# Optimization experiments

Measured on AMD Instinct MI355X. Metric: run time of the kernel, lower is better.

## Reference

```python
import jax, jax.numpy as jnp
import numpy as np

B, N, H = 2, 2048, 256
NUM_HEADS = 8
HEAD_DIM = H // NUM_HEADS
E = 65536
NEG = -1e30
LN_EPS = 1e-5


def setup_inputs() -> dict:
    key = jax.random.key(0)
    ks = jax.random.split(key, 8)
    x = jax.random.normal(ks[0], (B, N, H), dtype=jnp.float32)
    edge_index = jax.random.randint(ks[1], (2, E), 0, N, dtype=jnp.int32)
    edge_weights = jax.random.uniform(ks[2], (E,), dtype=jnp.float32)
    s = 1.0 / np.sqrt(H)
    Wq = jax.random.normal(ks[3], (H, H), dtype=jnp.float32) * s
    Wk = jax.random.normal(ks[4], (H, H), dtype=jnp.float32) * s
    Wv = jax.random.normal(ks[5], (H, H), dtype=jnp.float32) * s
    Wo = jax.random.normal(ks[6], (H, H), dtype=jnp.float32) * s
    ln_gamma = jnp.ones((H,), dtype=jnp.float32)
    ln_beta = jnp.zeros((H,), dtype=jnp.float32)
    return {"node_embeddings": x, "edge_index": edge_index, "edge_weights": edge_weights,
            "Wq": Wq, "Wk": Wk, "Wv": Wv, "Wo": Wo, "ln_gamma": ln_gamma, "ln_beta": ln_beta}


def reference(node_embeddings, edge_index, edge_weights, Wq, Wk, Wv, Wo, ln_gamma, ln_beta):
    x = node_embeddings
    residual = x
    # torch Linear: y = x @ W.T
    def proj(W):
        y = jnp.einsum('bnd,ed->bne', x, W)
        return y.reshape(B, N, NUM_HEADS, HEAD_DIM).transpose(0, 2, 1, 3)  # [B,h,N,hd]
    Q, K, V = proj(Wq), proj(Wk), proj(Wv)
    scale = 1.0 / jnp.sqrt(jnp.float32(HEAD_DIM))
    scores = jnp.einsum('bhnd,bhmd->bhnm', Q, K) * scale  # [B,h,N,N]
    # adjacency mask from edge list
    mask = jnp.zeros((N, N), dtype=bool).at[edge_index[0], edge_index[1]].set(True)
    scores = jnp.where(mask[None, None], scores, NEG)
    w = jax.nn.softmax(scores, axis=-1)
    # rows with no edges: softmax over uniform NEG -> uniform; multiply by mask zeroes them
    # (equivalent to torch's -inf softmax + nan->0, but grad-safe)
    w = w * mask[None, None].astype(w.dtype)
    attn = jnp.einsum('bhnm,bhmd->bhnd', w, V)
    attn = attn.transpose(0, 2, 1, 3).reshape(B, N, H)
    out = jnp.einsum('bnd,ed->bne', attn, Wo)
    y = out + residual
    mu = jnp.mean(y, axis=-1, keepdims=True)
    var = jnp.mean(jnp.square(y - mu), axis=-1, keepdims=True)
    y = (y - mu) / jnp.sqrt(var + LN_EPS) * ln_gamma + ln_beta
    return y
```

## Files before the change

### kernel.cpp

```cpp
#include <hip/hip_runtime.h>
#include <math.h>

#define Bb 2
#define Nn 2048
#define Hh 256
#define NH 8
#define HD 32
#define NEDGE 65536
#define LN_EPS 1e-5f
#define MW 64

typedef __bf16 bf16_t;
typedef bf16_t bf16x8 __attribute__((ext_vector_type(8)));
typedef bf16_t bf16x4 __attribute__((ext_vector_type(4)));
typedef float f32x4 __attribute__((ext_vector_type(4)));

__global__ void build_mask_kernel(const int* __restrict__ ei, unsigned int* __restrict__ mask) {
    int e = blockIdx.x * blockDim.x + threadIdx.x;
    if (e >= NEDGE) return;
    int src = ei[e];
    int dst = ei[NEDGE + e];
    atomicOr(&mask[src * MW + (dst >> 5)], 1u << (dst & 31));
}

#define LDA2 72

__global__ __launch_bounds__(256) void qkv_gemm3_kernel(
    const float* __restrict__ x,
    const float* __restrict__ Wq, const float* __restrict__ Wk, const float* __restrict__ Wv,
    float* __restrict__ Qb, bf16_t* __restrict__ Kb16, bf16_t* __restrict__ Vb16)
{
    __shared__ bf16_t As[64 * LDA2];
    __shared__ bf16_t Ws[64 * LDA2];
    int t = threadIdx.x;
    int lane = t & 63, w = t >> 6;
    int wm = w & 1, wn = w >> 1;
    int ml = lane & 15, quad = lane >> 4;
    int m0 = blockIdx.x * 64;
    int wsel = blockIdx.y >> 2;
    const float* W = (wsel == 0) ? Wq : ((wsel == 1) ? Wk : Wv);
    int n0 = (blockIdx.y & 3) * 64;
    int srow = t >> 3;
    int scol = (t & 7) * 8;
    f32x4 acc[2][2];
    f32x4 zero = {0.f, 0.f, 0.f, 0.f};
    acc[0][0] = zero; acc[0][1] = zero; acc[1][0] = zero; acc[1][1] = zero;

    for (int k0 = 0; k0 < Hh; k0 += 64) {
        float4 a[2][2], bwt[2][2];
        #pragma unroll
        for (int s = 0; s < 2; ++s) {
            const float* ap = x + (size_t)(m0 + srow + s * 32) * Hh + k0 + scol;
            a[s][0] = *(const float4*)ap;
            a[s][1] = *(const float4*)(ap + 4);
            const float* bp = W + (size_t)(n0 + srow + s * 32) * Hh + k0 + scol;
            bwt[s][0] = *(const float4*)bp;
            bwt[s][1] = *(const float4*)(bp + 4);
        }
        __syncthreads();
        #pragma unroll
        for (int s = 0; s < 2; ++s) {
            bf16x8 av = {(bf16_t)a[s][0].x, (bf16_t)a[s][0].y, (bf16_t)a[s][0].z, (bf16_t)a[s][0].w,
                         (bf16_t)a[s][1].x, (bf16_t)a[s][1].y, (bf16_t)a[s][1].z, (bf16_t)a[s][1].w};
            bf16x8 bv = {(bf16_t)bwt[s][0].x, (bf16_t)bwt[s][0].y, (bf16_t)bwt[s][0].z, (bf16_t)bwt[s][0].w,
                         (bf16_t)bwt[s][1].x, (bf16_t)bwt[s][1].y, (bf16_t)bwt[s][1].z, (bf16_t)bwt[s][1].w};
            *(bf16x8*)&As[(srow + s * 32) * LDA2 + scol] = av;
            *(bf16x8*)&Ws[(srow + s * 32) * LDA2 + scol] = bv;
        }
        __syncthreads();
        #pragma unroll
        for (int kk = 0; kk < 64; kk += 32) {
            bf16x8 af[2], bfr[2];
            #pragma unroll
            for (int i = 0; i < 2; ++i) {
                af[i]  = *(const bf16x8*)&As[(wm * 32 + i * 16 + ml) * LDA2 + kk + quad * 8];
                bfr[i] = *(const bf16x8*)&Ws[(wn * 32 + i * 16 + ml) * LDA2 + kk + quad * 8];
            }
            #pragma unroll
            for (int i = 0; i < 2; ++i)
                #pragma unroll
                for (int j = 0; j < 2; ++j)
                    acc[i][j] = __builtin_amdgcn_mfma_f32_16x16x32_bf16(af[i], bfr[j], acc[i][j], 0, 0, 0);
        }
    }
    bf16_t* Ob16 = (wsel == 1) ? Kb16 : Vb16;
    #pragma unroll
    for (int i = 0; i < 2; ++i)
        #pragma unroll
        for (int j = 0; j < 2; ++j)
            #pragma unroll
            for (int r = 0; r < 4; ++r) {
                int mg = m0 + wm * 32 + i * 16 + quad * 4 + r;
                int ng = n0 + wn * 32 + j * 16 + ml;
                float v = acc[i][j][r];
                if (wsel == 0) Qb[(size_t)mg * Hh + ng] = v;
                else           Ob16[(size_t)mg * Hh + ng] = (bf16_t)v;
            }
}

__global__ __launch_bounds__(256) void attn6_kernel(
    const float* __restrict__ Qb, const bf16_t* __restrict__ Kb16, const bf16_t* __restrict__ Vb16,
    const unsigned int* __restrict__ mask, float* __restrict__ attnb)
{
    __shared__ unsigned short nbr[Nn];
    __shared__ float qs[2][Hh];
    __shared__ float sraw[2][32 * 9];
    __shared__ float scw[2][Hh];
    __shared__ float alpha_l[2][NH];
    __shared__ float linv_l[2][NH];
    __shared__ float obuf[4][Hh];
    __shared__ int nn_sh;
    int i = blockIdx.x;
    int t = threadIdx.x;
    int h = t >> 5, dl = t & 31;
    int w = t >> 6, lane = t & 63;
    int hw = lane >> 3;

    if (t < 64) {
        unsigned int bits = mask[i * MW + t];
        int cnt = __popc(bits);
        int incl = cnt;
        #pragma unroll
        for (int off = 1; off < 64; off <<= 1) {
            int v = __shfl_up(incl, off, 64);
            if (t >= off) incl += v;
        }
        int idx = incl - cnt;
        unsigned int bb = bits;
        while (bb) {
            int bit = __ffs(bb) - 1;
            nbr[idx++] = (unsigned short)(t * 32 + bit);
            bb &= bb - 1;
        }
        if (t == 63) nn_sh = incl;
    }
    qs[0][t] = Qb[(size_t)i * Hh + t];
    qs[1][t] = Qb[(size_t)(Nn + i) * Hh + t];
    __syncthreads();
    int nn = nn_sh;

    float m_run[2] = {-1e30f, -1e30f};
    float l_run[2] = {0.f, 0.f};
    float o[2][4] = {{0.f, 0.f, 0.f, 0.f}, {0.f, 0.f, 0.f, 0.f}};
    const float scale = 0.17677669529663687f;
    int nch = (nn + 31) >> 5;
    for (int c = 0; c < nch; ++c) {
        int base = c << 5;
        int lim = min(32, nn - base);
        #pragma unroll
        for (int b = 0; b < 2; ++b) {
            float4 qv = *(const float4*)&qs[b][lane << 2];
            #pragma unroll
            for (int s = 0; s < 8; ++s) {
                int r = (s << 2) + w;
                if (r < lim) {
                    int j = nbr[base + r];
                    bf16x4 kv = *(const bf16x4*)(Kb16 + (((size_t)((b << 11) + j)) << 8) + (lane << 2));
                    float p = fmaf((float)kv.x, qv.x, fmaf((float)kv.y, qv.y,
                              fmaf((float)kv.z, qv.z, (float)kv.w * qv.w)));
                    p += __shfl_xor(p, 1, 64);
                    p += __shfl_xor(p, 2, 64);
                    p += __shfl_xor(p, 4, 64);
                    if ((lane & 7) == 0) sraw[b][r * 9 + (lane >> 3)] = p * scale;
                }
            }
        }
        __syncthreads();
        #pragma unroll
        for (int b = 0; b < 2; ++b) {
            float s_val = (dl < lim) ? sraw[b][dl * 9 + h] : -1e30f;
            float mc = s_val;
            #pragma unroll
            for (int m = 1; m < 32; m <<= 1) mc = fmaxf(mc, __shfl_xor(mc, m, 64));
            float m_new = fmaxf(m_run[b], mc);
            float wgt = __expf(s_val - m_new);
            float sum = wgt;
            #pragma unroll
            for (int m = 1; m < 32; m <<= 1) sum += __shfl_xor(sum, m, 64);
            float alpha = __expf(m_run[b] - m_new);
            l_run[b] = l_run[b] * alpha + sum;
            m_run[b] = m_new;
            scw[b][t] = wgt;
            if (dl == 0) alpha_l[b][h] = alpha;
        }
        __syncthreads();
        #pragma unroll
        for (int b = 0; b < 2; ++b) {
            float av = alpha_l[b][hw];
            o[b][0] *= av; o[b][1] *= av; o[b][2] *= av; o[b][3] *= av;
            #pragma unroll
            for (int s = 0; s < 8; ++s) {
                int r = (s << 2) + w;
                if (r < lim) {
                    int j = nbr[base + r];
                    float wg = scw[b][(hw << 5) + r];
                    bf16x4 vv = *(const bf16x4*)(Vb16 + (((size_t)((b << 11) + j)) << 8) + (lane << 2));
                    o[b][0] = fmaf(wg, (float)vv.x, o[b][0]);
                    o[b][1] = fmaf(wg, (float)vv.y, o[b][1]);
                    o[b][2] = fmaf(wg, (float)vv.z, o[b][2]);
                    o[b][3] = fmaf(wg, (float)vv.w, o[b][3]);
                }
            }
        }
    }
    if (dl == 0) {
        linv_l[0][h] = (l_run[0] > 0.f) ? 1.f / l_run[0] : 0.f;
        linv_l[1][h] = (l_run[1] > 0.f) ? 1.f / l_run[1] : 0.f;
    }
    #pragma unroll
    for (int b = 0; b < 2; ++b) {
        __syncthreads();
        obuf[w][(lane << 2) + 0] = o[b][0];
        obuf[w][(lane << 2) + 1] = o[b][1];
        obuf[w][(lane << 2) + 2] = o[b][2];
        obuf[w][(lane << 2) + 3] = o[b][3];
        __syncthreads();
        float val = obuf[0][t] + obuf[1][t] + obuf[2][t] + obuf[3][t];
        attnb[(((size_t)((b << 11) + i)) << 8) + t] = val * linv_l[b][t >> 5];
    }
}

__global__ __launch_bounds__(256) void out_ln_kernel(
    const float* __restrict__ attnb, const float* __restrict__ Wo,
    const float* __restrict__ x, const float* __restrict__ gamma,
    const float* __restrict__ beta, float* __restrict__ out)
{
    __shared__ bf16_t As[16 * LDA2];
    __shared__ __align__(16) char wbuf[256 * LDA2 * sizeof(bf16_t)];
    bf16_t* Ws = (bf16_t*)wbuf;
    float* yb = (float*)wbuf;
    int t = threadIdx.x;
    int lane = t & 63, w = t >> 6;
    int ml = lane & 15, quad = lane >> 4;
    int m0 = blockIdx.x * 16;
    f32x4 acc[4];
    f32x4 zero = {0.f, 0.f, 0.f, 0.f};
    acc[0] = zero; acc[1] = zero; acc[2] = zero; acc[3] = zero;
    int arow = t >> 4, acol = (t & 15) * 4;
    int wrow = t >> 3, wcol = (t & 7) * 8;

    for (int k0 = 0; k0 < Hh; k0 += 64) {
        float4 av = *(const float4*)(attnb + (size_t)(m0 + arow) * Hh + k0 + acol);
        float4 wva[8], wvb[8];
        #pragma unroll
        for (int s = 0; s < 8; ++s) {
            const float* wp = Wo + (size_t)(wrow + s * 32) * Hh + k0 + wcol;
            wva[s] = *(const float4*)wp;
            wvb[s] = *(const float4*)(wp + 4);
        }
        __syncthreads();
        bf16x4 ac = {(bf16_t)av.x, (bf16_t)av.y, (bf16_t)av.z, (bf16_t)av.w};
        *(bf16x4*)&As[arow * LDA2 + acol] = ac;
        #pragma unroll
        for (int s = 0; s < 8; ++s) {
            bf16x8 wv8 = {(bf16_t)wva[s].x, (bf16_t)wva[s].y, (bf16_t)wva[s].z, (bf16_t)wva[s].w,
                          (bf16_t)wvb[s].x, (bf16_t)wvb[s].y, (bf16_t)wvb[s].z, (bf16_t)wvb[s].w};
            *(bf16x8*)&Ws[(wrow + s * 32) * LDA2 + wcol] = wv8;
        }
        __syncthreads();
        #pragma unroll
        for (int kk = 0; kk < 64; kk += 32) {
            bf16x8 af = *(const bf16x8*)&As[ml * LDA2 + kk + quad * 8];
            #pragma unroll
            for (int ct = 0; ct < 4; ++ct) {
                bf16x8 bfr = *(const bf16x8*)&Ws[(w * 64 + ct * 16 + ml) * LDA2 + kk + quad * 8];
                acc[ct] = __builtin_amdgcn_mfma_f32_16x16x32_bf16(af, bfr, acc[ct], 0, 0, 0);
            }
        }
    }
    __syncthreads();
    #pragma unroll
    for (int ct = 0; ct < 4; ++ct)
        #pragma unroll
        for (int r = 0; r < 4; ++r) {
            int row = quad * 4 + r;
            int col = w * 64 + ct * 16 + ml;
            yb[row * 260 + col] = acc[ct][r] + x[(size_t)(m0 + row) * Hh + col];
        }
    __syncthreads();
    for (int rr = 0; rr < 4; ++rr) {
        int row = w * 4 + rr;
        float4 v = *(const float4*)&yb[row * 260 + lane * 4];
        float sum = v.x + v.y + v.z + v.w;
        #pragma unroll
        for (int m = 1; m < 64; m <<= 1) sum += __shfl_xor(sum, m, 64);
        float mu = sum * (1.f / Hh);
        float4 d = {v.x - mu, v.y - mu, v.z - mu, v.w - mu};
        float ss = d.x * d.x + d.y * d.y + d.z * d.z + d.w * d.w;
        #pragma unroll
        for (int m = 1; m < 64; m <<= 1) ss += __shfl_xor(ss, m, 64);
        float r = rsqrtf(ss * (1.f / Hh) + LN_EPS);
        float4 g  = *(const float4*)(gamma + lane * 4);
        float4 bt = *(const float4*)(beta + lane * 4);
        float4 ov = {d.x * r * g.x + bt.x, d.y * r * g.y + bt.y,
                     d.z * r * g.z + bt.z, d.w * r * g.w + bt.w};
        *(float4*)(out + (size_t)(m0 + row) * Hh + lane * 4) = ov;
    }
}

extern "C" void kernel_launch(void* const* d_in, const int* in_sizes, int n_in,
                              void* d_out, int out_size, void* d_ws, size_t ws_size,
                              hipStream_t stream) {
    const float* x     = (const float*)d_in[0];
    const int*   ei    = (const int*)d_in[1];
    const float* Wq    = (const float*)d_in[3];
    const float* Wk    = (const float*)d_in[4];
    const float* Wv    = (const float*)d_in[5];
    const float* Wo    = (const float*)d_in[6];
    const float* gamma = (const float*)d_in[7];
    const float* beta  = (const float*)d_in[8];
    float* out = (float*)d_out;

    const int NTOK = Bb * Nn * Hh;
    float*  Qb    = (float*)d_ws;
    bf16_t* Kb16  = (bf16_t*)(Qb + NTOK);
    bf16_t* Vb16  = Kb16 + NTOK;
    float*  attnb = (float*)(Vb16 + NTOK);
    unsigned int* mask = (unsigned int*)(attnb + NTOK);

    hipMemsetAsync(mask, 0, Nn * MW * sizeof(unsigned int), stream);
    hipLaunchKernelGGL(build_mask_kernel, dim3(NEDGE / 256), dim3(256), 0, stream, ei, mask);
    hipLaunchKernelGGL(qkv_gemm3_kernel, dim3((Bb * Nn) / 64, 12), dim3(256), 0, stream,
                       x, Wq, Wk, Wv, Qb, Kb16, Vb16);
    hipLaunchKernelGGL(attn6_kernel, dim3(Nn), dim3(256), 0, stream,
                       Qb, Kb16, Vb16, mask, attnb);
    hipLaunchKernelGGL(out_ln_kernel, dim3((Bb * Nn) / 16), dim3(256), 0, stream,
                       attnb, Wo, x, gamma, beta, out);
}
```

Baseline: 118.6 us.

## Fuse all stages into one persistent cooperative kernel with grid syncs

Adds a single persistent cooperative kernel that runs mask clearing, mask build plus QKV GEMM, sparse attention, and output projection with LayerNorm in sequence, separated by grid-wide syncs. It replaces the memset and four separate launches. The goal is to remove launch gaps and per-kernel tail effects. In exchange, grid size is capped by occupancy, each phase loops over work units, and the grid barriers add sync cost. The fallback path also changes the attention launch grid to Bb*Nn blocks, which looks inconsistent with the fused version's per-node loop over both batches.

```diff
diff --git a/kernel.cpp b/kernel.cpp
--- a/kernel.cpp
+++ b/kernel.cpp
@@ -1,5 +1,8 @@
 #include <hip/hip_runtime.h>
+#include <hip/hip_cooperative_groups.h>
 #include <math.h>
+
+namespace cg = cooperative_groups;
 
 #define Bb 2
 #define Nn 2048
@@ -9,11 +12,304 @@
 #define NEDGE 65536
 #define LN_EPS 1e-5f
 #define MW 64
+#define LDA2 72
 
 typedef __bf16 bf16_t;
 typedef bf16_t bf16x8 __attribute__((ext_vector_type(8)));
 typedef bf16_t bf16x4 __attribute__((ext_vector_type(4)));
 typedef float f32x4 __attribute__((ext_vector_type(4)));
+
+__global__ __launch_bounds__(256, 4) void fused_kernel(
+    const float* __restrict__ x, const int* __restrict__ ei,
+    const float* __restrict__ Wq, const float* __restrict__ Wk, const float* __restrict__ Wv,
+    const float* __restrict__ Wo, const float* __restrict__ gamma, const float* __restrict__ beta,
+    float* __restrict__ Qb, bf16_t* __restrict__ Kb16, bf16_t* __restrict__ Vb16,
+    float* __restrict__ attnb, unsigned int* __restrict__ mask, float* __restrict__ out)
+{
+    __shared__ __align__(16) char smembuf[39168];
+    cg::grid_group grid = cg::this_grid();
+    const int t = threadIdx.x;
+    const int bid = blockIdx.x;
+    const int g = gridDim.x;
+    const int lane = t & 63, w = t >> 6;
+    const int ml = lane & 15, quad = lane >> 4;
+
+    {
+        uint4* m4 = (uint4*)mask;
+        const uint4 z = make_uint4(0, 0, 0, 0);
+        for (int idx = bid * 256 + t; idx < Nn * MW / 4; idx += g * 256)
+            m4[idx] = z;
+    }
+    grid.sync();
+
+    {
+        bf16_t* As = (bf16_t*)smembuf;
+        bf16_t* Ws = (bf16_t*)(smembuf + 9216);
+        const int wm = w & 1, wn = w >> 1;
+        const int srow = t >> 3, scol = (t & 7) * 8;
+        for (int u = bid; u < 1024; u += g) {
+            if (u < 768) {
+                int m0 = (u & 63) << 6;
+                int ysel = u >> 6;
+                int wsel = ysel >> 2;
+                const float* W = (wsel == 0) ? Wq : ((wsel == 1) ? Wk : Wv);
+                int n0 = (ysel & 3) << 6;
+                f32x4 acc[2][2];
+                f32x4 zero = {0.f, 0.f, 0.f, 0.f};
+                acc[0][0] = zero; acc[0][1] = zero; acc[1][0] = zero; acc[1][1] = zero;
+                for (int k0 = 0; k0 < Hh; k0 += 64) {
+                    float4 a[2][2], bwt[2][2];
+                    #pragma unroll
+                    for (int s = 0; s < 2; ++s) {
+                        const float* ap = x + (size_t)(m0 + srow + s * 32) * Hh + k0 + scol;
+                        a[s][0] = *(const float4*)ap;
+                        a[s][1] = *(const float4*)(ap + 4);
+                        const float* bp = W + (size_t)(n0 + srow + s * 32) * Hh + k0 + scol;
+                        bwt[s][0] = *(const float4*)bp;
+                        bwt[s][1] = *(const float4*)(bp + 4);
+                    }
+                    __syncthreads();
+                    #pragma unroll
+                    for (int s = 0; s < 2; ++s) {
+                        bf16x8 av = {(bf16_t)a[s][0].x, (bf16_t)a[s][0].y, (bf16_t)a[s][0].z, (bf16_t)a[s][0].w,
+                                     (bf16_t)a[s][1].x, (bf16_t)a[s][1].y, (bf16_t)a[s][1].z, (bf16_t)a[s][1].w};
+                        bf16x8 bv = {(bf16_t)bwt[s][0].x, (bf16_t)bwt[s][0].y, (bf16_t)bwt[s][0].z, (bf16_t)bwt[s][0].w,
+                                     (bf16_t)bwt[s][1].x, (bf16_t)bwt[s][1].y, (bf16_t)bwt[s][1].z, (bf16_t)bwt[s][1].w};
+                        *(bf16x8*)&As[(srow + s * 32) * LDA2 + scol] = av;
+                        *(bf16x8*)&Ws[(srow + s * 32) * LDA2 + scol] = bv;
+                    }
+                    __syncthreads();
+                    #pragma unroll
+                    for (int kk = 0; kk < 64; kk += 32) {
+                        bf16x8 af[2], bfr[2];
+                        #pragma unroll
+                        for (int i2 = 0; i2 < 2; ++i2) {
+                            af[i2]  = *(const bf16x8*)&As[(wm * 32 + i2 * 16 + ml) * LDA2 + kk + quad * 8];
+                            bfr[i2] = *(const bf16x8*)&Ws[(wn * 32 + i2 * 16 + ml) * LDA2 + kk + quad * 8];
+                        }
+                        #pragma unroll
+                        for (int i2 = 0; i2 < 2; ++i2)
+                            #pragma unroll
+                            for (int j2 = 0; j2 < 2; ++j2)
+                                acc[i2][j2] = __builtin_amdgcn_mfma_f32_16x16x32_bf16(af[i2], bfr[j2], acc[i2][j2], 0, 0, 0);
+                    }
+                }
+                bf16_t* Ob16 = (wsel == 1) ? Kb16 : Vb16;
+                #pragma unroll
+                for (int i2 = 0; i2 < 2; ++i2)
+                    #pragma unroll
+                    for (int j2 = 0; j2 < 2; ++j2)
+                        #pragma unroll
+                        for (int r = 0; r < 4; ++r) {
+                            int mg = m0 + wm * 32 + i2 * 16 + quad * 4 + r;
+                            int ng = n0 + wn * 32 + j2 * 16 + ml;
+                            float v = acc[i2][j2][r];
+                            if (wsel == 0) Qb[(size_t)mg * Hh + ng] = v;
+                            else           Ob16[(size_t)mg * Hh + ng] = (bf16_t)v;
+                        }
+            } else {
+                int e = (u - 768) * 256 + t;
+                int src = ei[e];
+                int dst = ei[NEDGE + e];
+                atomicOr(&mask[src * MW + (dst >> 5)], 1u << (dst & 31));
+            }
+        }
+    }
+    __threadfence();
+    grid.sync();
+
+    {
+        unsigned short* nbr = (unsigned short*)smembuf;
+        float* qs      = (float*)(smembuf + 4096);
+        float* sraw    = (float*)(smembuf + 6144);
+        float* scw     = (float*)(smembuf + 8448);
+        float* alpha_l = (float*)(smembuf + 10496);
+        float* linv_l  = (float*)(smembuf + 10560);
+        float* obuf    = (float*)(smembuf + 10624);
+        int*   nn_sh   = (int*)(smembuf + 14720);
+        const int h = t >> 5, dl = t & 31;
+        const int hw = lane >> 3;
+        const float scale = 0.17677669529663687f;
+
+        for (int i = bid; i < Nn; i += g) {
+            if (t < 64) {
+                unsigned int bits = mask[i * MW + t];
+                int cnt = __popc(bits);
+                int incl = cnt;
+                #pragma unroll
+                for (int off = 1; off < 64; off <<= 1) {
+                    int v = __shfl_up(incl, off, 64);
+                    if (t >= off) incl += v;
+                }
+                int idx = incl - cnt;
+                unsigned int bb = bits;
+                while (bb) {
+                    int bit = __ffs(bb) - 1;
+                    nbr[idx++] = (unsigned short)(t * 32 + bit);
+                    bb &= bb - 1;
+                }
+                if (t == 63) *nn_sh = incl;
+            }
+            qs[t]       = Qb[(size_t)i * Hh + t];
+            qs[256 + t] = Qb[(size_t)(Nn + i) * Hh + t];
+            __syncthreads();
+            int nn = *nn_sh;
+
+            float m_run[2] = {-1e30f, -1e30f};
+            float l_run[2] = {0.f, 0.f};
+            float o[2][4] = {{0.f, 0.f, 0.f, 0.f}, {0.f, 0.f, 0.f, 0.f}};
+            int nch = (nn + 31) >> 5;
+            for (int c = 0; c < nch; ++c) {
+                int base = c << 5;
+                int lim = min(32, nn - base);
+                #pragma unroll
+                for (int b = 0; b < 2; ++b) {
+                    float4 qv = *(const float4*)&qs[b * 256 + (lane << 2)];
+                    #pragma unroll
+                    for (int s = 0; s < 8; ++s) {
+                        int r = (s << 2) + w;
+                        if (r < lim) {
+                            int j = nbr[base + r];
+                            bf16x4 kv = *(const bf16x4*)(Kb16 + (((size_t)((b << 11) + j)) << 8) + (lane << 2));
+                            float p = fmaf((float)kv.x, qv.x, fmaf((float)kv.y, qv.y,
+                                      fmaf((float)kv.z, qv.z, (float)kv.w * qv.w)));
+                            p += __shfl_xor(p, 1, 64);
+                            p += __shfl_xor(p, 2, 64);
+                            p += __shfl_xor(p, 4, 64);
+                            if ((lane & 7) == 0) sraw[b * 288 + r * 9 + (lane >> 3)] = p * scale;
+                        }
+                    }
+                }
+                __syncthreads();
+                #pragma unroll
+                for (int b = 0; b < 2; ++b) {
+                    float s_val = (dl < lim) ? sraw[b * 288 + dl * 9 + h] : -1e30f;
+                    float mc = s_val;
+                    #pragma unroll
+                    for (int m = 1; m < 32; m <<= 1) mc = fmaxf(mc, __shfl_xor(mc, m, 64));
+                    float m_new = fmaxf(m_run[b], mc);
+                    float wgt = __expf(s_val - m_new);
+                    float sum = wgt;
+                    #pragma unroll
+                    for (int m = 1; m < 32; m <<= 1) sum += __shfl_xor(sum, m, 64);
+                    float alpha = __expf(m_run[b] - m_new);
+                    l_run[b] = l_run[b] * alpha + sum;
+                    m_run[b] = m_new;
+                    scw[b * 256 + t] = wgt;
+                    if (dl == 0) alpha_l[b * 8 + h] = alpha;
+                }
+                __syncthreads();
+                #pragma unroll
+                for (int b = 0; b < 2; ++b) {
+                    float av = alpha_l[b * 8 + hw];
+                    o[b][0] *= av; o[b][1] *= av; o[b][2] *= av; o[b][3] *= av;
+                    #pragma unroll
+                    for (int s = 0; s < 8; ++s) {
+                        int r = (s << 2) + w;
+                        if (r < lim) {
+                            int j = nbr[base + r];
+                            float wg = scw[b * 256 + (hw << 5) + r];
+                            bf16x4 vv = *(const bf16x4*)(Vb16 + (((size_t)((b << 11) + j)) << 8) + (lane << 2));
+                            o[b][0] = fmaf(wg, (float)vv.x, o[b][0]);
+                            o[b][1] = fmaf(wg, (float)vv.y, o[b][1]);
+                            o[b][2] = fmaf(wg, (float)vv.z, o[b][2]);
+                            o[b][3] = fmaf(wg, (float)vv.w, o[b][3]);
+                        }
+                    }
+                }
+            }
+            if (dl == 0) {
+                linv_l[h]     = (l_run[0] > 0.f) ? 1.f / l_run[0] : 0.f;
+                linv_l[8 + h] = (l_run[1] > 0.f) ? 1.f / l_run[1] : 0.f;
+            }
+            #pragma unroll
+            for (int b = 0; b < 2; ++b) {
+                __syncthreads();
+                obuf[w * 256 + (lane << 2) + 0] = o[b][0];
+                obuf[w * 256 + (lane << 2) + 1] = o[b][1];
+                obuf[w * 256 + (lane << 2) + 2] = o[b][2];
+                obuf[w * 256 + (lane << 2) + 3] = o[b][3];
+                __syncthreads();
+                float val = obuf[t] + obuf[256 + t] + obuf[512 + t] + obuf[768 + t];
+                attnb[(((size_t)((b << 11) + i)) << 8) + t] = val * linv_l[b * 8 + (t >> 5)];
+            }
+        }
+    }
+    __threadfence();
+    grid.sync();
+
+    {
+        bf16_t* As = (bf16_t*)smembuf;
+        bf16_t* Ws = (bf16_t*)(smembuf + 2304);
+        float*  yb = (float*)(smembuf + 2304);
+        const int arow = t >> 4, acol = (t & 15) * 4;
+        const int wrow = t >> 3, wcol = (t & 7) * 8;
+        for (int u = bid; u < (Bb * Nn) / 16; u += g) {
+            int m0 = u * 16;
+            f32x4 acc[4];
+            f32x4 zero = {0.f, 0.f, 0.f, 0.f};
+            acc[0] = zero; acc[1] = zero; acc[2] = zero; acc[3] = zero;
+            for (int k0 = 0; k0 < Hh; k0 += 64) {
+                float4 av = *(const float4*)(attnb + (size_t)(m0 + arow) * Hh + k0 + acol);
+                float4 wva[8], wvb[8];
+                #pragma unroll
+                for (int s = 0; s < 8; ++s) {
+                    const float* wp = Wo + (size_t)(wrow + s * 32) * Hh + k0 + wcol;
+                    wva[s] = *(const float4*)wp;
+                    wvb[s] = *(const float4*)(wp + 4);
+                }
+                __syncthreads();
+                bf16x4 ac = {(bf16_t)av.x, (bf16_t)av.y, (bf16_t)av.z, (bf16_t)av.w};
+                *(bf16x4*)&As[arow * LDA2 + acol] = ac;
+                #pragma unroll
+                for (int s = 0; s < 8; ++s) {
+                    bf16x8 wv8 = {(bf16_t)wva[s].x, (bf16_t)wva[s].y, (bf16_t)wva[s].z, (bf16_t)wva[s].w,
+                                  (bf16_t)wvb[s].x, (bf16_t)wvb[s].y, (bf16_t)wvb[s].z, (bf16_t)wvb[s].w};
+                    *(bf16x8*)&Ws[(wrow + s * 32) * LDA2 + wcol] = wv8;
+                }
+                __syncthreads();
+                #pragma unroll
+                for (int kk = 0; kk < 64; kk += 32) {
+                    bf16x8 af = *(const bf16x8*)&As[ml * LDA2 + kk + quad * 8];
+                    #pragma unroll
+                    for (int ct = 0; ct < 4; ++ct) {
+                        bf16x8 bfr = *(const bf16x8*)&Ws[(w * 64 + ct * 16 + ml) * LDA2 + kk + quad * 8];
+                        acc[ct] = __builtin_amdgcn_mfma_f32_16x16x32_bf16(af, bfr, acc[ct], 0, 0, 0);
+                    }
+                }
+            }
+            __syncthreads();
+            #pragma unroll
+            for (int ct = 0; ct < 4; ++ct)
+                #pragma unroll
+                for (int r = 0; r < 4; ++r) {
+                    int row = quad * 4 + r;
+                    int col = w * 64 + ct * 16 + ml;
+                    yb[row * 260 + col] = acc[ct][r] + x[(size_t)(m0 + row) * Hh + col];
+                }
+            __syncthreads();
+            for (int rr = 0; rr < 4; ++rr) {
+                int row = w * 4 + rr;
+                float4 v = *(const float4*)&yb[row * 260 + lane * 4];
+                float sum = v.x + v.y + v.z + v.w;
+                #pragma unroll
+                for (int m = 1; m < 64; m <<= 1) sum += __shfl_xor(sum, m, 64);
+                float mu = sum * (1.f / Hh);
+                float4 d = {v.x - mu, v.y - mu, v.z - mu, v.w - mu};
+                float ss = d.x * d.x + d.y * d.y + d.z * d.z + d.w * d.w;
+                #pragma unroll
+                for (int m = 1; m < 64; m <<= 1) ss += __shfl_xor(ss, m, 64);
+                float r = rsqrtf(ss * (1.f / Hh) + LN_EPS);
+                float4 gmv = *(const float4*)(gamma + lane * 4);
+                float4 btv = *(const float4*)(beta + lane * 4);
+                float4 ov = {d.x * r * gmv.x + btv.x, d.y * r * gmv.y + btv.y,
+                             d.z * r * gmv.z + btv.z, d.w * r * gmv.w + btv.w};
+                *(float4*)(out + (size_t)(m0 + row) * Hh + lane * 4) = ov;
+            }
+            __syncthreads();
+        }
+    }
+}
 
 __global__ void build_mask_kernel(const int* __restrict__ ei, unsigned int* __restrict__ mask) {
     int e = blockIdx.x * blockDim.x + threadIdx.x;
@@ -22,8 +318,6 @@
     int dst = ei[NEDGE + e];
     atomicOr(&mask[src * MW + (dst >> 5)], 1u << (dst & 31));
 }
-
-#define LDA2 72
 
 __global__ __launch_bounds__(256) void qkv_gemm3_kernel(
     const float* __restrict__ x,
@@ -318,11 +612,41 @@
     float*  attnb = (float*)(Vb16 + NTOK);
     unsigned int* mask = (unsigned int*)(attnb + NTOK);
 
+    static int coop_blocks = -2;
+    if (coop_blocks == -2) {
+        int per_cu = 0;
+        hipError_t e = hipOccupancyMaxActiveBlocksPerMultiprocessor(&per_cu, fused_kernel, 256, 0);
+        if (e != hipSuccess || per_cu <= 0) {
+            coop_blocks = 0;
+        } else {
+            int num_cu = 256;
+            hipDeviceProp_t prop;
+            int dev = 0;
+            if (hipGetDevice(&dev) == hipSuccess && hipGetDeviceProperties(&prop, dev) == hipSuccess)
+                num_cu = prop.multiProcessorCount;
+            long cap = (long)per_cu * num_cu;
+            coop_blocks = (int)(cap < 1024 ? cap : 1024);
+        }
+    }
+
+    if (coop_blocks > 0) {
+        void* args[] = {
+            (void*)&x, (void*)&ei, (void*)&Wq, (void*)&Wk, (void*)&Wv,
+            (void*)&Wo, (void*)&gamma, (void*)&beta,
+            (void*)&Qb, (void*)&Kb16, (void*)&Vb16,
+            (void*)&attnb, (void*)&mask, (void*)&out};
+        hipError_t e = hipLaunchCooperativeKernel((const void*)fused_kernel,
+                                                  dim3(coop_blocks), dim3(256),
+                                                  args, 0, stream);
+        if (e == hipSuccess) return;
+        coop_blocks = 0;
+    }
+
     hipMemsetAsync(mask, 0, Nn * MW * sizeof(unsigned int), stream);
     hipLaunchKernelGGL(build_mask_kernel, dim3(NEDGE / 256), dim3(256), 0, stream, ei, mask);
     hipLaunchKernelGGL(qkv_gemm3_kernel, dim3((Bb * Nn) / 64, 12), dim3(256), 0, stream,
                        x, Wq, Wk, Wv, Qb, Kb16, Vb16);
-    hipLaunchKernelGGL(attn6_kernel, dim3(Nn), dim3(256), 0, stream,
+    hipLaunchKernelGGL(attn6_kernel, dim3(Bb * Nn), dim3(256), 0, stream,
                        Qb, Kb16, Vb16, mask, attnb);
     hipLaunchKernelGGL(out_ln_kernel, dim3((Bb * Nn) / 16), dim3(256), 0, stream,
                        attnb, Wo, x, gamma, beta, out);
```

Result: slower. 434.0 us (+265.8%).

## Fuse output projection and LayerNorm into attention kernel; merge mask clear and Wo cast into prep

Applied to the files above, without the earlier changes.

The output projection with Wo, the residual add and the LayerNorm now run at the end of the attention kernel, so the fp32 attention intermediate is never written to or read from global memory. The memset and a pre-cast of Wo to bf16 are folded into the QKV GEMM launch as extra blocks, which removes one launch and the separate memset. The price is that each attention block runs a 2-row MFMA with 14 of 16 rows zero-padded and reads all of Wo from global/L2 per block, which wastes MFMA throughput and adds L2 traffic.

```diff
diff --git a/kernel.cpp b/kernel.cpp
--- a/kernel.cpp
+++ b/kernel.cpp
@@ -9,39 +9,50 @@
 #define NEDGE 65536
 #define LN_EPS 1e-5f
 #define MW 64
+#define LDA2 72
 
 typedef __bf16 bf16_t;
 typedef bf16_t bf16x8 __attribute__((ext_vector_type(8)));
 typedef bf16_t bf16x4 __attribute__((ext_vector_type(4)));
 typedef float f32x4 __attribute__((ext_vector_type(4)));
 
-__global__ void build_mask_kernel(const int* __restrict__ ei, unsigned int* __restrict__ mask) {
-    int e = blockIdx.x * blockDim.x + threadIdx.x;
-    if (e >= NEDGE) return;
-    int src = ei[e];
-    int dst = ei[NEDGE + e];
-    atomicOr(&mask[src * MW + (dst >> 5)], 1u << (dst & 31));
-}
-
-#define LDA2 72
-
-__global__ __launch_bounds__(256) void qkv_gemm3_kernel(
+__global__ __launch_bounds__(256) void prep_kernel(
     const float* __restrict__ x,
     const float* __restrict__ Wq, const float* __restrict__ Wk, const float* __restrict__ Wv,
-    float* __restrict__ Qb, bf16_t* __restrict__ Kb16, bf16_t* __restrict__ Vb16)
+    const float* __restrict__ Wo,
+    float* __restrict__ Qb, bf16_t* __restrict__ Kb16, bf16_t* __restrict__ Vb16,
+    bf16_t* __restrict__ Wob, unsigned int* __restrict__ mask)
 {
     __shared__ bf16_t As[64 * LDA2];
     __shared__ bf16_t Ws[64 * LDA2];
-    int t = threadIdx.x;
-    int lane = t & 63, w = t >> 6;
-    int wm = w & 1, wn = w >> 1;
-    int ml = lane & 15, quad = lane >> 4;
-    int m0 = blockIdx.x * 64;
-    int wsel = blockIdx.y >> 2;
+    const int u = blockIdx.x;
+    const int t = threadIdx.x;
+
+    if (u >= 768) {
+        if (u < 800) {
+            uint4* m4 = (uint4*)mask;
+            const uint4 z = make_uint4(0, 0, 0, 0);
+            int b0 = (u - 768) * 1024 + t;
+            #pragma unroll
+            for (int r = 0; r < 4; ++r) m4[b0 + r * 256] = z;
+        } else {
+            int i = (u - 800) * 256 + t;
+            float4 v = ((const float4*)Wo)[i];
+            bf16x4 o = {(bf16_t)v.x, (bf16_t)v.y, (bf16_t)v.z, (bf16_t)v.w};
+            ((bf16x4*)Wob)[i] = o;
+        }
+        return;
+    }
+
+    const int lane = t & 63, w = t >> 6;
+    const int wm = w & 1, wn = w >> 1;
+    const int ml = lane & 15, quad = lane >> 4;
+    const int m0 = (u & 63) << 6;
+    const int ysel = u >> 6;
+    const int wsel = ysel >> 2;
     const float* W = (wsel == 0) ? Wq : ((wsel == 1) ? Wk : Wv);
-    int n0 = (blockIdx.y & 3) * 64;
-    int srow = t >> 3;
-    int scol = (t & 7) * 8;
+    const int n0 = (ysel & 3) << 6;
+    const int srow = t >> 3, scol = (t & 7) * 8;
     f32x4 acc[2][2];
     f32x4 zero = {0.f, 0.f, 0.f, 0.f};
     acc[0][0] = zero; acc[0][1] = zero; acc[1][0] = zero; acc[1][1] = zero;
@@ -98,23 +109,36 @@
             }
 }
 
-__global__ __launch_bounds__(256) void attn6_kernel(
+__global__ void build_mask_kernel(const int* __restrict__ ei, unsigned int* __restrict__ mask) {
+    int e = blockIdx.x * blockDim.x + threadIdx.x;
+    if (e >= NEDGE) return;
+    int src = ei[e];
+    int dst = ei[NEDGE + e];
+    atomicOr(&mask[src * MW + (dst >> 5)], 1u << (dst & 31));
+}
+
+__global__ __launch_bounds__(256) void attn_fused_kernel(
     const float* __restrict__ Qb, const bf16_t* __restrict__ Kb16, const bf16_t* __restrict__ Vb16,
-    const unsigned int* __restrict__ mask, float* __restrict__ attnb)
+    const unsigned int* __restrict__ mask, const bf16_t* __restrict__ Wob,
+    const float* __restrict__ x, const float* __restrict__ gamma, const float* __restrict__ beta,
+    float* __restrict__ out)
 {
     __shared__ unsigned short nbr[Nn];
     __shared__ float qs[2][Hh];
-    __shared__ float sraw[2][32 * 9];
+    __shared__ float sraw[2][288];
     __shared__ float scw[2][Hh];
     __shared__ float alpha_l[2][NH];
     __shared__ float linv_l[2][NH];
     __shared__ float obuf[4][Hh];
+    __shared__ bf16_t aLDS[2 * Hh];
+    __shared__ float ybuf[2][Hh];
     __shared__ int nn_sh;
-    int i = blockIdx.x;
-    int t = threadIdx.x;
-    int h = t >> 5, dl = t & 31;
-    int w = t >> 6, lane = t & 63;
-    int hw = lane >> 3;
+    const int i = blockIdx.x;
+    const int t = threadIdx.x;
+    const int h = t >> 5, dl = t & 31;
+    const int w = t >> 6, lane = t & 63;
+    const int ml = lane & 15, quad = lane >> 4;
+    const int hw = lane >> 3;
 
     if (t < 64) {
         unsigned int bits = mask[i * MW + t];
@@ -215,72 +239,42 @@
         obuf[w][(lane << 2) + 2] = o[b][2];
         obuf[w][(lane << 2) + 3] = o[b][3];
         __syncthreads();
-        float val = obuf[0][t] + obuf[1][t] + obuf[2][t] + obuf[3][t];
-        attnb[(((size_t)((b << 11) + i)) << 8) + t] = val * linv_l[b][t >> 5];
-    }
-}
-
-__global__ __launch_bounds__(256) void out_ln_kernel(
-    const float* __restrict__ attnb, const float* __restrict__ Wo,
-    const float* __restrict__ x, const float* __restrict__ gamma,
-    const float* __restrict__ beta, float* __restrict__ out)
-{
-    __shared__ bf16_t As[16 * LDA2];
-    __shared__ __align__(16) char wbuf[256 * LDA2 * sizeof(bf16_t)];
-    bf16_t* Ws = (bf16_t*)wbuf;
-    float* yb = (float*)wbuf;
-    int t = threadIdx.x;
-    int lane = t & 63, w = t >> 6;
-    int ml = lane & 15, quad = lane >> 4;
-    int m0 = blockIdx.x * 16;
-    f32x4 acc[4];
-    f32x4 zero = {0.f, 0.f, 0.f, 0.f};
-    acc[0] = zero; acc[1] = zero; acc[2] = zero; acc[3] = zero;
-    int arow = t >> 4, acol = (t & 15) * 4;
-    int wrow = t >> 3, wcol = (t & 7) * 8;
-
-    for (int k0 = 0; k0 < Hh; k0 += 64) {
-        float4 av = *(const float4*)(attnb + (size_t)(m0 + arow) * Hh + k0 + acol);
-        float4 wva[8], wvb[8];
-        #pragma unroll
-        for (int s = 0; s < 8; ++s) {
-            const float* wp = Wo + (size_t)(wrow + s * 32) * Hh + k0 + wcol;
-            wva[s] = *(const float4*)wp;
-            wvb[s] = *(const float4*)(wp + 4);
-        }
-        __syncthreads();
-        bf16x4 ac = {(bf16_t)av.x, (bf16_t)av.y, (bf16_t)av.z, (bf16_t)av.w};
-        *(bf16x4*)&As[arow * LDA2 + acol] = ac;
-        #pragma unroll
-        for (int s = 0; s < 8; ++s) {
-            bf16x8 wv8 = {(bf16_t)wva[s].x, (bf16_t)wva[s].y, (bf16_t)wva[s].z, (bf16_t)wva[s].w,
-                          (bf16_t)wvb[s].x, (bf16_t)wvb[s].y, (bf16_t)wvb[s].z, (bf16_t)wvb[s].w};
-            *(bf16x8*)&Ws[(wrow + s * 32) * LDA2 + wcol] = wv8;
-        }
-        __syncthreads();
-        #pragma unroll
-        for (int kk = 0; kk < 64; kk += 32) {
-            bf16x8 af = *(const bf16x8*)&As[ml * LDA2 + kk + quad * 8];
-            #pragma unroll
-            for (int ct = 0; ct < 4; ++ct) {
-                bf16x8 bfr = *(const bf16x8*)&Ws[(w * 64 + ct * 16 + ml) * LDA2 + kk + quad * 8];
-                acc[ct] = __builtin_amdgcn_mfma_f32_16x16x32_bf16(af, bfr, acc[ct], 0, 0, 0);
-            }
-        }
+        float val = (obuf[0][t] + obuf[1][t] + obuf[2][t] + obuf[3][t]) * linv_l[b][t >> 5];
+        aLDS[(b << 8) + t] = (bf16_t)val;
     }
     __syncthreads();
+
+    f32x4 pacc[4];
+    {
+        f32x4 pz = {0.f, 0.f, 0.f, 0.f};
+        pacc[0] = pz; pacc[1] = pz; pacc[2] = pz; pacc[3] = pz;
+    }
+    const bf16x8 zero8 = {(bf16_t)0.f, (bf16_t)0.f, (bf16_t)0.f, (bf16_t)0.f,
+                          (bf16_t)0.f, (bf16_t)0.f, (bf16_t)0.f, (bf16_t)0.f};
     #pragma unroll
-    for (int ct = 0; ct < 4; ++ct)
-        #pragma unroll
-        for (int r = 0; r < 4; ++r) {
-            int row = quad * 4 + r;
+    for (int k8 = 0; k8 < 8; ++k8) {
+        bf16x8 af = zero8;
+        if (ml < 2) af = *(const bf16x8*)&aLDS[(ml << 8) + k8 * 32 + quad * 8];
+        #pragma unroll
+        for (int ct = 0; ct < 4; ++ct) {
+            const bf16_t* bp = Wob + (size_t)(w * 64 + ct * 16 + ml) * Hh + k8 * 32 + quad * 8;
+            bf16x8 bfr = *(const bf16x8*)bp;
+            pacc[ct] = __builtin_amdgcn_mfma_f32_16x16x32_bf16(af, bfr, pacc[ct], 0, 0, 0);
+        }
+    }
+    if (quad == 0) {
+        #pragma unroll
+        for (int ct = 0; ct < 4; ++ct) {
             int col = w * 64 + ct * 16 + ml;
-            yb[row * 260 + col] = acc[ct][r] + x[(size_t)(m0 + row) * Hh + col];
-        }
+            #pragma unroll
+            for (int r = 0; r < 2; ++r)
+                ybuf[r][col] = pacc[ct][r] + x[(size_t)((r << 11) + i) * Hh + col];
+        }
+    }
     __syncthreads();
-    for (int rr = 0; rr < 4; ++rr) {
-        int row = w * 4 + rr;
-        float4 v = *(const float4*)&yb[row * 260 + lane * 4];
+
+    if (w < 2) {
+        float4 v = *(const float4*)&ybuf[w][lane << 2];
         float sum = v.x + v.y + v.z + v.w;
         #pragma unroll
         for (int m = 1; m < 64; m <<= 1) sum += __shfl_xor(sum, m, 64);
@@ -290,11 +284,11 @@
         #pragma unroll
         for (int m = 1; m < 64; m <<= 1) ss += __shfl_xor(ss, m, 64);
         float r = rsqrtf(ss * (1.f / Hh) + LN_EPS);
-        float4 g  = *(const float4*)(gamma + lane * 4);
-        float4 bt = *(const float4*)(beta + lane * 4);
+        float4 g  = *(const float4*)(gamma + (lane << 2));
+        float4 bt = *(const float4*)(beta + (lane << 2));
         float4 ov = {d.x * r * g.x + bt.x, d.y * r * g.y + bt.y,
                      d.z * r * g.z + bt.z, d.w * r * g.w + bt.w};
-        *(float4*)(out + (size_t)(m0 + row) * Hh + lane * 4) = ov;
+        *(float4*)(out + (size_t)((w << 11) + i) * Hh + (lane << 2)) = ov;
     }
 }
 
@@ -315,15 +309,12 @@
     float*  Qb    = (float*)d_ws;
     bf16_t* Kb16  = (bf16_t*)(Qb + NTOK);
     bf16_t* Vb16  = Kb16 + NTOK;
-    float*  attnb = (float*)(Vb16 + NTOK);
-    unsigned int* mask = (unsigned int*)(attnb + NTOK);
-
-    hipMemsetAsync(mask, 0, Nn * MW * sizeof(unsigned int), stream);
+    unsigned int* mask = (unsigned int*)(Vb16 + NTOK);
+    bf16_t* Wob   = (bf16_t*)(mask + Nn * MW);
+
+    hipLaunchKernelGGL(prep_kernel, dim3(864), dim3(256), 0, stream,
+                       x, Wq, Wk, Wv, Wo, Qb, Kb16, Vb16, Wob, mask);
     hipLaunchKernelGGL(build_mask_kernel, dim3(NEDGE / 256), dim3(256), 0, stream, ei, mask);
-    hipLaunchKernelGGL(qkv_gemm3_kernel, dim3((Bb * Nn) / 64, 12), dim3(256), 0, stream,
-                       x, Wq, Wk, Wv, Qb, Kb16, Vb16);
-    hipLaunchKernelGGL(attn6_kernel, dim3(Nn), dim3(256), 0, stream,
-                       Qb, Kb16, Vb16, mask, attnb);
-    hipLaunchKernelGGL(out_ln_kernel, dim3((Bb * Nn) / 16), dim3(256), 0, stream,
-                       attnb, Wo, x, gamma, beta, out);
+    hipLaunchKernelGGL(attn_fused_kernel, dim3(Nn), dim3(256), 0, stream,
+                       Qb, Kb16, Vb16, mask, Wob, x, gamma, beta, out);
 }
```

Result: slower. 144.7 us (+22.0%).

## Fold mask zeroing into QKV kernel and restructure attention to one wave per row-batch

Applied to the files above, without the earlier changes.

The mask memset is replaced by extra blocks in the QKV GEMM launch that zero the bitmask, removing one stream operation. The attention kernel now assigns each wave one (row, batch) pair and runs a per-neighbor online softmax entirely in registers with software-prefetched K/V loads. This removes the chunked shared-memory staging, block-wide syncs and cross-wave reductions. The cost is a serial per-neighbor dependency chain with two exps per neighbor, and each wave rebuilds its own neighbor list.

```diff
diff --git a/kernel.cpp b/kernel.cpp
--- a/kernel.cpp
+++ b/kernel.cpp
@@ -9,39 +9,42 @@
 #define NEDGE 65536
 #define LN_EPS 1e-5f
 #define MW 64
+#define LDA2 72
 
 typedef __bf16 bf16_t;
 typedef bf16_t bf16x8 __attribute__((ext_vector_type(8)));
 typedef bf16_t bf16x4 __attribute__((ext_vector_type(4)));
 typedef float f32x4 __attribute__((ext_vector_type(4)));
 
-__global__ void build_mask_kernel(const int* __restrict__ ei, unsigned int* __restrict__ mask) {
-    int e = blockIdx.x * blockDim.x + threadIdx.x;
-    if (e >= NEDGE) return;
-    int src = ei[e];
-    int dst = ei[NEDGE + e];
-    atomicOr(&mask[src * MW + (dst >> 5)], 1u << (dst & 31));
-}
-
-#define LDA2 72
-
-__global__ __launch_bounds__(256) void qkv_gemm3_kernel(
+__global__ __launch_bounds__(256) void prep_kernel(
     const float* __restrict__ x,
     const float* __restrict__ Wq, const float* __restrict__ Wk, const float* __restrict__ Wv,
-    float* __restrict__ Qb, bf16_t* __restrict__ Kb16, bf16_t* __restrict__ Vb16)
+    float* __restrict__ Qb, bf16_t* __restrict__ Kb16, bf16_t* __restrict__ Vb16,
+    unsigned int* __restrict__ mask)
 {
     __shared__ bf16_t As[64 * LDA2];
     __shared__ bf16_t Ws[64 * LDA2];
-    int t = threadIdx.x;
-    int lane = t & 63, w = t >> 6;
-    int wm = w & 1, wn = w >> 1;
-    int ml = lane & 15, quad = lane >> 4;
-    int m0 = blockIdx.x * 64;
-    int wsel = blockIdx.y >> 2;
+    const int u = blockIdx.x;
+    const int t = threadIdx.x;
+
+    if (u >= 768) {
+        uint4* m4 = (uint4*)mask;
+        const uint4 z = make_uint4(0, 0, 0, 0);
+        int b0 = (u - 768) * 1024 + t;
+        #pragma unroll
+        for (int r = 0; r < 4; ++r) m4[b0 + r * 256] = z;
+        return;
+    }
+
+    const int lane = t & 63, w = t >> 6;
+    const int wm = w & 1, wn = w >> 1;
+    const int ml = lane & 15, quad = lane >> 4;
+    const int m0 = (u & 63) << 6;
+    const int ysel = u >> 6;
+    const int wsel = ysel >> 2;
     const float* W = (wsel == 0) ? Wq : ((wsel == 1) ? Wk : Wv);
-    int n0 = (blockIdx.y & 3) * 64;
-    int srow = t >> 3;
-    int scol = (t & 7) * 8;
+    const int n0 = (ysel & 3) << 6;
+    const int srow = t >> 3, scol = (t & 7) * 8;
     f32x4 acc[2][2];
     f32x4 zero = {0.f, 0.f, 0.f, 0.f};
     acc[0][0] = zero; acc[0][1] = zero; acc[1][0] = zero; acc[1][1] = zero;
@@ -98,126 +101,80 @@
             }
 }
 
-__global__ __launch_bounds__(256) void attn6_kernel(
+__global__ void build_mask_kernel(const int* __restrict__ ei, unsigned int* __restrict__ mask) {
+    int e = blockIdx.x * blockDim.x + threadIdx.x;
+    if (e >= NEDGE) return;
+    int src = ei[e];
+    int dst = ei[NEDGE + e];
+    atomicOr(&mask[src * MW + (dst >> 5)], 1u << (dst & 31));
+}
+
+__global__ __launch_bounds__(256) void attn7_kernel(
     const float* __restrict__ Qb, const bf16_t* __restrict__ Kb16, const bf16_t* __restrict__ Vb16,
     const unsigned int* __restrict__ mask, float* __restrict__ attnb)
 {
-    __shared__ unsigned short nbr[Nn];
-    __shared__ float qs[2][Hh];
-    __shared__ float sraw[2][32 * 9];
-    __shared__ float scw[2][Hh];
-    __shared__ float alpha_l[2][NH];
-    __shared__ float linv_l[2][NH];
-    __shared__ float obuf[4][Hh];
-    __shared__ int nn_sh;
-    int i = blockIdx.x;
-    int t = threadIdx.x;
-    int h = t >> 5, dl = t & 31;
-    int w = t >> 6, lane = t & 63;
-    int hw = lane >> 3;
-
-    if (t < 64) {
-        unsigned int bits = mask[i * MW + t];
-        int cnt = __popc(bits);
-        int incl = cnt;
-        #pragma unroll
-        for (int off = 1; off < 64; off <<= 1) {
-            int v = __shfl_up(incl, off, 64);
-            if (t >= off) incl += v;
-        }
-        int idx = incl - cnt;
-        unsigned int bb = bits;
-        while (bb) {
-            int bit = __ffs(bb) - 1;
-            nbr[idx++] = (unsigned short)(t * 32 + bit);
-            bb &= bb - 1;
-        }
-        if (t == 63) nn_sh = incl;
-    }
-    qs[0][t] = Qb[(size_t)i * Hh + t];
-    qs[1][t] = Qb[(size_t)(Nn + i) * Hh + t];
+    __shared__ unsigned short nbr[4][2048];
+    const int t = threadIdx.x;
+    const int w = t >> 6, lane = t & 63;
+    const int i = (blockIdx.x << 1) + (w >> 1);
+    const int b = w & 1;
+
+    unsigned int bits = mask[i * MW + lane];
+    int cnt = __popc(bits);
+    int incl = cnt;
+    #pragma unroll
+    for (int off = 1; off < 64; off <<= 1) {
+        int v = __shfl_up(incl, off, 64);
+        if (lane >= off) incl += v;
+    }
+    int idx = incl - cnt;
+    unsigned int bb = bits;
+    while (bb) {
+        int bit = __ffs(bb) - 1;
+        nbr[w][idx++] = (unsigned short)(lane * 32 + bit);
+        bb &= bb - 1;
+    }
+    int nn = __shfl(incl, 63, 64);
+    if (lane == 63) nbr[w][idx] = 0;
     __syncthreads();
-    int nn = nn_sh;
-
-    float m_run[2] = {-1e30f, -1e30f};
-    float l_run[2] = {0.f, 0.f};
-    float o[2][4] = {{0.f, 0.f, 0.f, 0.f}, {0.f, 0.f, 0.f, 0.f}};
+
+    const int off4 = lane << 2;
+    const float4 qv = *(const float4*)(Qb + (size_t)((b << 11) + i) * Hh + off4);
+    const bf16_t* kb = Kb16 + (((size_t)(b << 11)) << 8);
+    const bf16_t* vb = Vb16 + (((size_t)(b << 11)) << 8);
     const float scale = 0.17677669529663687f;
-    int nch = (nn + 31) >> 5;
-    for (int c = 0; c < nch; ++c) {
-        int base = c << 5;
-        int lim = min(32, nn - base);
-        #pragma unroll
-        for (int b = 0; b < 2; ++b) {
-            float4 qv = *(const float4*)&qs[b][lane << 2];
-            #pragma unroll
-            for (int s = 0; s < 8; ++s) {
-                int r = (s << 2) + w;
-                if (r < lim) {
-                    int j = nbr[base + r];
-                    bf16x4 kv = *(const bf16x4*)(Kb16 + (((size_t)((b << 11) + j)) << 8) + (lane << 2));
-                    float p = fmaf((float)kv.x, qv.x, fmaf((float)kv.y, qv.y,
-                              fmaf((float)kv.z, qv.z, (float)kv.w * qv.w)));
-                    p += __shfl_xor(p, 1, 64);
-                    p += __shfl_xor(p, 2, 64);
-                    p += __shfl_xor(p, 4, 64);
-                    if ((lane & 7) == 0) sraw[b][r * 9 + (lane >> 3)] = p * scale;
-                }
-            }
-        }
-        __syncthreads();
-        #pragma unroll
-        for (int b = 0; b < 2; ++b) {
-            float s_val = (dl < lim) ? sraw[b][dl * 9 + h] : -1e30f;
-            float mc = s_val;
-            #pragma unroll
-            for (int m = 1; m < 32; m <<= 1) mc = fmaxf(mc, __shfl_xor(mc, m, 64));
-            float m_new = fmaxf(m_run[b], mc);
-            float wgt = __expf(s_val - m_new);
-            float sum = wgt;
-            #pragma unroll
-            for (int m = 1; m < 32; m <<= 1) sum += __shfl_xor(sum, m, 64);
-            float alpha = __expf(m_run[b] - m_new);
-            l_run[b] = l_run[b] * alpha + sum;
-            m_run[b] = m_new;
-            scw[b][t] = wgt;
-            if (dl == 0) alpha_l[b][h] = alpha;
-        }
-        __syncthreads();
-        #pragma unroll
-        for (int b = 0; b < 2; ++b) {
-            float av = alpha_l[b][hw];
-            o[b][0] *= av; o[b][1] *= av; o[b][2] *= av; o[b][3] *= av;
-            #pragma unroll
-            for (int s = 0; s < 8; ++s) {
-                int r = (s << 2) + w;
-                if (r < lim) {
-                    int j = nbr[base + r];
-                    float wg = scw[b][(hw << 5) + r];
-                    bf16x4 vv = *(const bf16x4*)(Vb16 + (((size_t)((b << 11) + j)) << 8) + (lane << 2));
-                    o[b][0] = fmaf(wg, (float)vv.x, o[b][0]);
-                    o[b][1] = fmaf(wg, (float)vv.y, o[b][1]);
-                    o[b][2] = fmaf(wg, (float)vv.z, o[b][2]);
-                    o[b][3] = fmaf(wg, (float)vv.w, o[b][3]);
-                }
-            }
-        }
-    }
-    if (dl == 0) {
-        linv_l[0][h] = (l_run[0] > 0.f) ? 1.f / l_run[0] : 0.f;
-        linv_l[1][h] = (l_run[1] > 0.f) ? 1.f / l_run[1] : 0.f;
-    }
-    #pragma unroll
-    for (int b = 0; b < 2; ++b) {
-        __syncthreads();
-        obuf[w][(lane << 2) + 0] = o[b][0];
-        obuf[w][(lane << 2) + 1] = o[b][1];
-        obuf[w][(lane << 2) + 2] = o[b][2];
-        obuf[w][(lane << 2) + 3] = o[b][3];
-        __syncthreads();
-        float val = obuf[0][t] + obuf[1][t] + obuf[2][t] + obuf[3][t];
-        attnb[(((size_t)((b << 11) + i)) << 8) + t] = val * linv_l[b][t >> 5];
-    }
+
+    float m_run = -1e30f, l_run = 0.f;
+    float o0 = 0.f, o1 = 0.f, o2 = 0.f, o3 = 0.f;
+    if (nn > 0) {
+        int j = nbr[w][0];
+        bf16x4 kv = *(const bf16x4*)(kb + ((size_t)j << 8) + off4);
+        bf16x4 vv = *(const bf16x4*)(vb + ((size_t)j << 8) + off4);
+        for (int n = 0; n < nn; ++n) {
+            int jn = nbr[w][n + 1];
+            bf16x4 kn = *(const bf16x4*)(kb + ((size_t)jn << 8) + off4);
+            bf16x4 vn = *(const bf16x4*)(vb + ((size_t)jn << 8) + off4);
+            float p = fmaf((float)kv.x, qv.x, fmaf((float)kv.y, qv.y,
+                      fmaf((float)kv.z, qv.z, (float)kv.w * qv.w)));
+            p += __shfl_xor(p, 1, 64);
+            p += __shfl_xor(p, 2, 64);
+            p += __shfl_xor(p, 4, 64);
+            p *= scale;
+            float m_new = fmaxf(m_run, p);
+            float alpha = __expf(m_run - m_new);
+            float wgt   = __expf(p - m_new);
+            l_run = fmaf(l_run, alpha, wgt);
+            o0 = fmaf(o0, alpha, wgt * (float)vv.x);
+            o1 = fmaf(o1, alpha, wgt * (float)vv.y);
+            o2 = fmaf(o2, alpha, wgt * (float)vv.z);
+            o3 = fmaf(o3, alpha, wgt * (float)vv.w);
+            m_run = m_new;
+            kv = kn; vv = vn;
+        }
+    }
+    float linv = (l_run > 0.f) ? 1.f / l_run : 0.f;
+    float4 ov = {o0 * linv, o1 * linv, o2 * linv, o3 * linv};
+    *(float4*)(attnb + ((size_t)((b << 11) + i) << 8) + off4) = ov;
 }
 
 __global__ __launch_bounds__(256) void out_ln_kernel(
@@ -318,11 +275,10 @@
     float*  attnb = (float*)(Vb16 + NTOK);
     unsigned int* mask = (unsigned int*)(attnb + NTOK);
 
-    hipMemsetAsync(mask, 0, Nn * MW * sizeof(unsigned int), stream);
+    hipLaunchKernelGGL(prep_kernel, dim3(800), dim3(256), 0, stream,
+                       x, Wq, Wk, Wv, Qb, Kb16, Vb16, mask);
     hipLaunchKernelGGL(build_mask_kernel, dim3(NEDGE / 256), dim3(256), 0, stream, ei, mask);
-    hipLaunchKernelGGL(qkv_gemm3_kernel, dim3((Bb * Nn) / 64, 12), dim3(256), 0, stream,
-                       x, Wq, Wk, Wv, Qb, Kb16, Vb16);
-    hipLaunchKernelGGL(attn6_kernel, dim3(Nn), dim3(256), 0, stream,
+    hipLaunchKernelGGL(attn7_kernel, dim3(Nn / 2), dim3(256), 0, stream,
                        Qb, Kb16, Vb16, mask, attnb);
     hipLaunchKernelGGL(out_ln_kernel, dim3((Bb * Nn) / 16), dim3(256), 0, stream,
                        attnb, Wo, x, gamma, beta, out);
```

Result: faster. 116.1 us (-2.1%).
